# Kernel tuning notes

Measured on AMD Instinct MI355X. Metric: run time of the kernel, lower is better.

The kernel has to match this reference:

```python
import jax, jax.numpy as jnp
import numpy as np


def _safe_norm(d):
    # Euclidean norm over last axis with torch-style subgradient 0 at 0
    sq = jnp.sum(d * d, axis=-1)
    pos = sq > 0
    return jnp.where(pos, jnp.sqrt(jnp.where(pos, sq, 1.0)), 0.0)


def setup_inputs() -> dict:
    key = jax.random.key(0)
    k1, k2 = jax.random.split(key)
    B, n = 8, 256
    src = jax.random.uniform(k1, (B, n, 2), dtype=jnp.float32) * 2.0 - 1.0
    dst = jax.random.uniform(k2, (B, n, 2), dtype=jnp.float32) * 2.0 - 1.0
    return {"src": src, "dst": dst, "s": 256}


def reference(src, dst, s):
    B, n, _ = src.shape
    dt = src.dtype
    # evaluation grid, matching torch.meshgrid(indexing='ij') then stack((ix,iy))
    lin = jnp.linspace(-1.0, 1.0, s, dtype=dt)
    iy, ix = jnp.meshgrid(lin, lin, indexing="ij")
    gs = jnp.stack((ix, iy), axis=2).reshape(1, -1, 2)  # (1, s*s, 2)

    # TPS system: L wv = rhs
    delta = src[:, :, None, :] - src[:, None, :, :]          # (B,n,n,2)
    K = _safe_norm(delta)                                     # (B,n,n)
    P = jnp.concatenate([jnp.ones((B, n, 1), dt), src], 2)    # (B,n,3)
    top = jnp.concatenate([K, P], 2)                          # (B,n,n+3)
    bot = jnp.concatenate([jnp.swapaxes(P, 1, 2),
                           jnp.zeros((B, 3, 3), dt)], 2)      # (B,3,n+3)
    L = jnp.concatenate([top, bot], 1)                        # (B,n+3,n+3)
    rhs = jnp.concatenate([dst, jnp.zeros((B, 3, 2), dt)], 1) # (B,n+3,2)
    wv = jnp.linalg.solve(L, rhs)                             # (B,n+3,2)

    # evaluate warp on the grid
    S = s * s
    dg = gs[:, :, None, :] - src[:, None, :, :]               # (B,S,n,2)
    Kg = _safe_norm(dg)                                       # (B,S,n)
    gsb = jnp.broadcast_to(gs, (B, S, 2))
    Pg = jnp.concatenate([jnp.ones((B, S, 1), dt), gsb], 2)   # (B,S,3)
    Lg = jnp.concatenate([Kg, Pg], 2)                         # (B,S,n+3)
    out = jnp.matmul(Lg, wv)                                  # (B,S,2)
    return out.reshape(B, s, s, 2).transpose(0, 3, 1, 2)
```

## Files before the change

### kernel.cpp

```cpp
#include <hip/hip_runtime.h>
#include <math.h>

#define NCTRL 256
#define NA    259
#define NAUG  261
#define APITCH 264
#define BATCH 8
#define SGRID 256
#define NB    32
#define NPAN  9
#define PPITCH 36

__global__ __launch_bounds__(256) void build_kernel(const float* __restrict__ src,
                                                    const float* __restrict__ dst,
                                                    float* __restrict__ A){
  const int b = blockIdx.x / 13;
  const int s = blockIdx.x - b*13;
  const int r0 = s*20;
  const int r1 = (r0 + 20 < NA) ? r0 + 20 : NA;
  const float* sb = src + b*NCTRL*2;
  const float* db = dst + b*NCTRL*2;
  float* Ab = A + (size_t)b*NA*APITCH;
  __shared__ float sx[NCTRL], sy[NCTRL];
  {
    int t = threadIdx.x;
    float2 v = ((const float2*)sb)[t];
    sx[t] = v.x; sy[t] = v.y;
  }
  __syncthreads();
  const int total = (r1 - r0)*APITCH;
  for (int idx = threadIdx.x; idx < total; idx += 256){
    int r = r0 + idx / APITCH;
    int c = idx % APITCH;
    float v = 0.0f;
    if (r < NCTRL){
      if (c < NCTRL){
        float dx = sx[r] - sx[c];
        float dy = sy[r] - sy[c];
        v = sqrtf(fmaf(dx, dx, dy*dy));
      } else if (c == NCTRL)   v = 1.0f;
      else if (c == NCTRL+1)   v = sx[r];
      else if (c == NCTRL+2)   v = sy[r];
      else if (c == NA)        v = db[2*r];
      else if (c == NA+1)      v = db[2*r+1];
    } else if (c < NCTRL){
      v = (r == NCTRL) ? 1.0f : ((r == NCTRL+1) ? sx[c] : sy[c]);
    }
    Ab[(size_t)r*APITCH + c] = v;
  }
}

template<int NBC, int NW>
__device__ __forceinline__ void panel_ministeps(
    float (&rr)[NBC], int& org, const int rows,
    const int tid, const int lane, const int wid,
    float (*redrow)[NW][PPITCH], float (*jrow)[PPITCH],
    float (*redv)[NW], int (*redi)[NW], int (*redo_)[NW], int* jorg)
{
  #pragma unroll
  for (int j = 0; j < NBC; ++j){
    const int par = j & 1;
    float bv = (tid >= j && tid < rows) ? fabsf(rr[j]) : -1.0f;
    int bi = tid;
    #pragma unroll
    for (int off = 32; off; off >>= 1){
      float ov = __shfl_xor(bv, off);
      int   oi = __shfl_xor(bi, off);
      if (ov > bv || (ov == bv && oi < bi)){ bv = ov; bi = oi; }
    }
    if (tid == bi){
      redv[par][wid] = bv; redi[par][wid] = bi; redo_[par][wid] = org;
      if (bv >= 0.0f){
        if (NBC == NB){
          #pragma unroll
          for (int q = 0; q < 8; ++q){
            float4 v; v.x=rr[4*q]; v.y=rr[4*q+1]; v.z=rr[4*q+2]; v.w=rr[4*q+3];
            *(float4*)&redrow[par][wid][4*q] = v;
          }
        } else {
          #pragma unroll
          for (int c = 0; c < NBC; ++c) redrow[par][wid][c] = rr[c];
        }
      }
    }
    if (tid == j){
      jorg[par] = org;
      if (NBC == NB){
        #pragma unroll
        for (int q = 0; q < 8; ++q){
          float4 v; v.x=rr[4*q]; v.y=rr[4*q+1]; v.z=rr[4*q+2]; v.w=rr[4*q+3];
          *(float4*)&jrow[par][4*q] = v;
        }
      } else {
        #pragma unroll
        for (int c = 0; c < NBC; ++c) jrow[par][c] = rr[c];
      }
    }
    __syncthreads();
    float gv = redv[par][0]; int gw = 0;
    #pragma unroll
    for (int w = 1; w < NW; ++w){
      if (redv[par][w] > gv ||
          (redv[par][w] == gv && redi[par][w] < redi[par][gw])){
        gv = redv[par][w]; gw = w;
      }
    }
    const int gbi  = redi[par][gw];
    const int gorg = redo_[par][gw];
    float pr[NBC];
    if (NBC == NB){
      #pragma unroll
      for (int q = 0; q < 8; ++q){
        float4 v = *(const float4*)&redrow[par][gw][4*q];
        pr[4*q]=v.x; pr[4*q+1]=v.y; pr[4*q+2]=v.z; pr[4*q+3]=v.w;
      }
    } else {
      #pragma unroll
      for (int c = 0; c < NBC; ++c) pr[c] = redrow[par][gw][c];
    }
    if (gbi != j){
      if (tid == j){
        #pragma unroll
        for (int c = 0; c < NBC; ++c) rr[c] = pr[c];
        org = gorg;
      } else if (tid == gbi){
        #pragma unroll
        for (int c = 0; c < NBC; ++c) rr[c] = jrow[par][c];
        org = jorg[par];
      }
    }
    if (tid > j && tid < rows){
      const float rpiv = 1.0f / pr[j];
      float f = rr[j] * rpiv;
      rr[j] = f;
      #pragma unroll
      for (int c = j+1; c < NBC; ++c) rr[c] = fmaf(-f, pr[c], rr[c]);
    }
  }
}

template<int NBC>
__global__ __launch_bounds__(320) void panel_kernel(float* __restrict__ A,
                                                    int* __restrict__ permbuf,
                                                    int k0, int pidx){
  const int b = blockIdx.x;
  float* Ab = A + (size_t)b*NA*APITCH;
  const int tid  = threadIdx.x;
  const int lane = tid & 63;
  const int wid  = tid >> 6;
  const int rows = NA - k0;

  __shared__ float pan[NA][PPITCH];
  __shared__ float redrow[2][5][PPITCH];
  __shared__ float jrow[2][PPITCH];
  __shared__ float redv[2][5];
  __shared__ int   redi[2][5], redo_[2][5];
  __shared__ int   jorg[2];

  for (int idx = tid; idx < rows*8; idx += 320){
    int i = idx >> 3, q = idx & 7;
    *(float4*)&pan[i][4*q] =
      *(const float4*)(Ab + (size_t)(k0+i)*APITCH + k0 + 4*q);
  }
  __syncthreads();

  float rr[NBC];
  int org = tid;
  if (tid < rows){
    #pragma unroll
    for (int q = 0; q < 8; ++q){
      float4 v = *(const float4*)&pan[tid][4*q];
      rr[4*q]=v.x; rr[4*q+1]=v.y; rr[4*q+2]=v.z; rr[4*q+3]=v.w;
    }
  } else {
    #pragma unroll
    for (int c = 0; c < NBC; ++c) rr[c] = 0.0f;
  }

  panel_ministeps<NBC,5>(rr, org, rows, tid, lane, wid,
                         redrow, jrow, redv, redi, redo_, jorg);

  if (tid < rows){
    #pragma unroll
    for (int q = 0; q < 8; ++q){
      float4 v; v.x=rr[4*q]; v.y=rr[4*q+1]; v.z=rr[4*q+2]; v.w=rr[4*q+3];
      *(float4*)&pan[tid][4*q] = v;
    }
    permbuf[b*(NPAN*NA) + pidx*NA + tid] = org;
  }
  __syncthreads();
  for (int idx = tid; idx < rows*8; idx += 320){
    int i = idx >> 3, q = idx & 7;
    *(float4*)(Ab + (size_t)(k0+i)*APITCH + k0 + 4*q) = *(const float4*)&pan[i][4*q];
  }
}

template<int NBC, int NBCN, bool LOOK>
__global__ __launch_bounds__(256) void update_kernel(float* __restrict__ A,
                                                     int* __restrict__ permbuf,
                                                     int k0, int pidx, int sb){
  const int rows = NA - k0;
  const int ctop = k0 + NBC;
  const int tc   = NAUG - ctop;
  const int b    = blockIdx.x / sb;
  const int s    = blockIdx.x - b*sb;
  const int c0   = s*32;
  const int W    = (tc - c0 < 32) ? (tc - c0) : 32;
  float* Ab = A + (size_t)b*NA*APITCH;
  const int tid  = threadIdx.x;
  const int lane = tid & 63;
  const int wid  = tid >> 6;

  __shared__ float pan[NA][PPITCH];
  __shared__ float stage[NA][PPITCH];
  __shared__ float ustg[NB][PPITCH];
  __shared__ int   perm[NA];
  __shared__ float redrowL[2][4][PPITCH];
  __shared__ float jrowL[2][PPITCH];
  __shared__ float redvL[2][4];
  __shared__ int   rediL[2][4], redoL[2][4];
  __shared__ int   jorgL[2];

  for (int i = tid; i < rows; i += 256)
    perm[i] = permbuf[b*(NPAN*NA) + pidx*NA + i];
  if (NBC == NB){
    for (int idx = tid; idx < rows*8; idx += 256){
      int i = idx >> 3, q = idx & 7;
      *(float4*)&pan[i][4*q] =
        *(const float4*)(Ab + (size_t)(k0+i)*APITCH + k0 + 4*q);
    }
  } else {
    for (int idx = tid; idx < rows*NBC; idx += 256){
      int i = idx / NBC, c = idx - i*NBC;
      pan[i][c] = Ab[(size_t)(k0+i)*APITCH + k0 + c];
    }
  }
  __syncthreads();

  for (int idx = tid; idx < rows*W; idx += 256){
    int i = idx / W, c = idx - i*W;
    stage[i][c] = Ab[(size_t)(k0+perm[i])*APITCH + ctop + c0 + c];
  }
  __syncthreads();

  if (tid < W){
    float u[NBC];
    #pragma unroll
    for (int m = 0; m < NBC; ++m) u[m] = stage[m][tid];
    #pragma unroll
    for (int m = 0; m < NBC; ++m){
      #pragma unroll
      for (int jj = m+1; jj < NBC; ++jj)
        u[jj] = fmaf(-pan[jj][m], u[m], u[jj]);
    }
    #pragma unroll
    for (int m = 0; m < NBC; ++m){
      ustg[m][tid] = u[m];
      Ab[(size_t)(k0+m)*APITCH + ctop + c0 + tid] = u[m];
    }
  }
  __syncthreads();

  const int R = rows - NBC;
  if (R > 0){
    const int rt = (R + 3) >> 2, ct = (W + 3) >> 2;
    for (int t = tid; t < rt*ct; t += 256){
      int tr = t / ct, tcc = t - tr*ct;
      int i0 = tr*4, cc0 = tcc*4;
      const bool full = (cc0 + 4 <= W);
      int ir[4];
      #pragma unroll
      for (int r = 0; r < 4; ++r){
        int i = i0 + r;
        ir[r] = (i < R) ? i : (R - 1);
      }
      float acc[4][4];
      #pragma unroll
      for (int r = 0; r < 4; ++r){
        if (full){
          float4 v = *(const float4*)&stage[NBC + ir[r]][cc0];
          acc[r][0]=v.x; acc[r][1]=v.y; acc[r][2]=v.z; acc[r][3]=v.w;
        } else {
          #pragma unroll
          for (int c = 0; c < 4; ++c)
            acc[r][c] = (cc0 + c < W) ? stage[NBC + ir[r]][cc0 + c] : 0.0f;
        }
      }
      if (NBC == NB){
        #pragma unroll
        for (int mq = 0; mq < NBC/4; ++mq){
          float4 lv[4];
          #pragma unroll
          for (int r = 0; r < 4; ++r)
            lv[r] = *(const float4*)&pan[NBC + ir[r]][4*mq];
          #pragma unroll
          for (int mi = 0; mi < 4; ++mi){
            float4 uv = *(const float4*)&ustg[4*mq + mi][cc0];
            #pragma unroll
            for (int r = 0; r < 4; ++r){
              float l = (mi==0) ? lv[r].x : (mi==1) ? lv[r].y : (mi==2) ? lv[r].z : lv[r].w;
              acc[r][0] = fmaf(-l, uv.x, acc[r][0]);
              acc[r][1] = fmaf(-l, uv.y, acc[r][1]);
              acc[r][2] = fmaf(-l, uv.z, acc[r][2]);
              acc[r][3] = fmaf(-l, uv.w, acc[r][3]);
            }
          }
        }
      } else {
        #pragma unroll
        for (int mi = 0; mi < NBC; ++mi){
          #pragma unroll
          for (int r = 0; r < 4; ++r){
            float l = pan[NBC + ir[r]][mi];
            #pragma unroll
            for (int c = 0; c < 4; ++c)
              acc[r][c] = fmaf(-l, ustg[mi][cc0 + c], acc[r][c]);
          }
        }
      }
      #pragma unroll
      for (int r = 0; r < 4; ++r){
        if (i0 + r < R){
          float* g = Ab + (size_t)(k0 + NBC + i0 + r)*APITCH + ctop + c0 + cc0;
          if (full){
            float4 v; v.x=acc[r][0]; v.y=acc[r][1]; v.z=acc[r][2]; v.w=acc[r][3];
            *(float4*)g = v;
            if (LOOK && s == 0) *(float4*)&stage[NBC + i0 + r][cc0] = v;
          } else {
            #pragma unroll
            for (int c = 0; c < 4; ++c)
              if (cc0 + c < W){
                g[c] = acc[r][c];
                if (LOOK && s == 0) stage[NBC + i0 + r][cc0 + c] = acc[r][c];
              }
          }
        }
      }
    }
  }

  if (LOOK && s == 0){
    __syncthreads();
    const int k0n   = k0 + NBC;
    const int rowsN = rows - NBC;
    float rr[NBCN];
    int org = tid;
    if (tid < rowsN){
      #pragma unroll
      for (int c = 0; c < NBCN; ++c) rr[c] = stage[NBC + tid][c];
    } else {
      #pragma unroll
      for (int c = 0; c < NBCN; ++c) rr[c] = 0.0f;
    }
    panel_ministeps<NBCN,4>(rr, org, rowsN, tid, lane, wid,
                            redrowL, jrowL, redvL, rediL, redoL, jorgL);
    if (tid < rowsN){
      #pragma unroll
      for (int c = 0; c < NBCN; ++c) stage[NBC + tid][c] = rr[c];
      permbuf[b*(NPAN*NA) + (pidx+1)*NA + tid] = org;
    }
    __syncthreads();
    if (NBCN == NB){
      for (int idx = tid; idx < rowsN*8; idx += 256){
        int i = idx >> 3, q = idx & 7;
        *(float4*)(Ab + (size_t)(k0n+i)*APITCH + k0n + 4*q) =
          *(const float4*)&stage[NBC + i][4*q];
      }
    } else {
      for (int idx = tid; idx < rowsN*NBCN; idx += 256){
        int i = idx / NBCN, c = idx - i*NBCN;
        Ab[(size_t)(k0n+i)*APITCH + k0n + c] = stage[NBC + i][c];
      }
    }
  }
}

__global__ __launch_bounds__(512) void backsub_kernel(const float* __restrict__ A,
                                                      float* __restrict__ wv){
  const int b = blockIdx.x;
  const float* Ab = A + (size_t)b*NA*APITCH;
  const int tid  = threadIdx.x;
  const int lane = tid & 63;
  const int wid  = tid >> 6;

  __shared__ float t2[NA][2];
  __shared__ float xs[NA][2];
  __shared__ float u11[NB][NB+1];

  for (int i = tid; i < NA; i += 512){
    t2[i][0] = Ab[(size_t)i*APITCH + NA];
    t2[i][1] = Ab[(size_t)i*APITCH + NA + 1];
  }
  __syncthreads();

  for (int bp = NPAN-1; bp >= 0; --bp){
    const int k0 = bp*NB;
    const int nb = (NA - k0 < NB) ? (NA - k0) : NB;

    for (int idx = tid; idx < nb*nb; idx += 512){
      int r = idx / nb, c = idx - r*nb;
      u11[r][c] = Ab[(size_t)(k0+r)*APITCH + k0 + c];
    }
    __syncthreads();

    if (wid == 0){
      int j = lane >> 1, ch = lane & 1;
      float tval = (j < nb) ? t2[k0+j][ch] : 0.0f;
      for (int k = nb-1; k >= 0; --k){
        float tk = __shfl(tval, 2*k + ch);
        float xk = tk / u11[k][k];
        if (j <  k) tval = fmaf(-u11[j][k], xk, tval);
        if (j == k) tval = xk;
      }
      if (j < nb) xs[k0+j][ch] = tval;
    }
    __syncthreads();

    if (nb == NB){
      const int q = tid & 7;
      for (int base = 0; base < k0; base += 64){
        const int i = base + (tid >> 3);
        float px = 0.0f, py = 0.0f;
        if (i < k0){
          float4 v = *(const float4*)(Ab + (size_t)i*APITCH + k0 + 4*q);
          px = v.x*xs[k0+4*q+0][0] + v.y*xs[k0+4*q+1][0]
             + v.z*xs[k0+4*q+2][0] + v.w*xs[k0+4*q+3][0];
          py = v.x*xs[k0+4*q+0][1] + v.y*xs[k0+4*q+1][1]
             + v.z*xs[k0+4*q+2][1] + v.w*xs[k0+4*q+3][1];
        }
        px += __shfl_xor(px, 1); px += __shfl_xor(px, 2); px += __shfl_xor(px, 4);
        py += __shfl_xor(py, 1); py += __shfl_xor(py, 2); py += __shfl_xor(py, 4);
        if (q == 0 && i < k0){
          t2[i][0] -= px;
          t2[i][1] -= py;
        }
      }
    } else {
      for (int i = tid; i < k0; i += 512){
        float s0 = 0.0f, s1 = 0.0f;
        #pragma unroll
        for (int m = 0; m < 3; ++m){
          float u = Ab[(size_t)i*APITCH + k0 + m];
          s0 = fmaf(u, xs[k0+m][0], s0);
          s1 = fmaf(u, xs[k0+m][1], s1);
        }
        t2[i][0] -= s0;
        t2[i][1] -= s1;
      }
    }
    __syncthreads();
  }

  for (int i = tid; i < NA; i += 512){
    wv[((size_t)b*NA + i)*2 + 0] = xs[i][0];
    wv[((size_t)b*NA + i)*2 + 1] = xs[i][1];
  }
}

__global__ __launch_bounds__(256) void eval_kernel(const float* __restrict__ src,
                                                   const float* __restrict__ wv,
                                                   float* __restrict__ out){
  const int b  = blockIdx.x >> 8;
  const int yi = blockIdx.x & 255;
  const int xi = threadIdx.x;
  __shared__ float2 sxy[NCTRL], wxy[NCTRL];
  const float* sb = src + b*NCTRL*2;
  const float* wb = wv + (size_t)b*NA*2;
  sxy[xi] = ((const float2*)sb)[xi];
  wxy[xi] = ((const float2*)wb)[xi];
  __syncthreads();

  const float step = 2.0f/255.0f;
  const float gx = -1.0f + step*(float)xi;
  const float gy = -1.0f + step*(float)yi;

  float accx = wb[512] + wb[514]*gx + wb[516]*gy;
  float accy = wb[513] + wb[515]*gx + wb[517]*gy;

  #pragma unroll 8
  for (int j = 0; j < NCTRL; ++j){
    float2 s = sxy[j];
    float2 w = wxy[j];
    float dx = gx - s.x;
    float dy = gy - s.y;
    float r = sqrtf(fmaf(dx, dx, dy*dy));
    accx = fmaf(r, w.x, accx);
    accy = fmaf(r, w.y, accy);
  }
  out[((size_t)(b*2    )*SGRID + yi)*SGRID + xi] = accx;
  out[((size_t)(b*2 + 1)*SGRID + yi)*SGRID + xi] = accy;
}

extern "C" void kernel_launch(void* const* d_in, const int* in_sizes, int n_in,
                              void* d_out, int out_size, void* d_ws, size_t ws_size,
                              hipStream_t stream) {
  const float* src = (const float*)d_in[0];
  const float* dst = (const float*)d_in[1];
  float* out = (float*)d_out;

  const size_t matElems = (size_t)BATCH*NA*APITCH;
  float* A     = (float*)d_ws;
  float* wv    = A + matElems;
  int*   permb = (int*)(wv + (size_t)BATCH*NA*2);

  build_kernel<<<BATCH*13, 256, 0, stream>>>(src, dst, A);

  panel_kernel<NB><<<BATCH, 320, 0, stream>>>(A, permb, 0, 0);

  for (int p = 0; p <= 6; ++p){
    const int k0 = p*NB;
    const int tc = NAUG - (k0 + NB);
    const int sb = (tc + 31) >> 5;
    update_kernel<NB, NB, true><<<BATCH*sb, 256, 0, stream>>>(A, permb, k0, p, sb);
  }
  update_kernel<NB, 3, true><<<BATCH, 256, 0, stream>>>(A, permb, 7*NB, 7, 1);
  update_kernel<3, 3, false><<<BATCH, 256, 0, stream>>>(A, permb, 8*NB, 8, 1);

  backsub_kernel<<<BATCH, 512, 0, stream>>>(A, wv);
  eval_kernel<<<BATCH*SGRID, 256, 0, stream>>>(src, wv, out);
}
```

Baseline: 595.4 us.

## Fuse build with first panel, move panel factorization to LDS, tile eval rows

Merges matrix construction and the first panel LU into one kernel, and rewrites the panel mini-step engine to operate on shared-memory rows instead of register arrays. The final 3-column panel is folded into the last lookahead update, which drops a launch. The eval kernel now computes four grid rows per thread, reusing dx and the control-point loads, and uses the hardware sqrt builtin. Together these cut launches and per-point ALU work. The costs are a single-block-per-batch build, so construction is less parallel, and extra LDS traffic in the panel loop.

```diff
diff --git a/kernel.cpp b/kernel.cpp
--- a/kernel.cpp
+++ b/kernel.cpp
@@ -10,57 +10,18 @@
 #define NB    32
 #define NPAN  9
 #define PPITCH 36
-
-__global__ __launch_bounds__(256) void build_kernel(const float* __restrict__ src,
-                                                    const float* __restrict__ dst,
-                                                    float* __restrict__ A){
-  const int b = blockIdx.x / 13;
-  const int s = blockIdx.x - b*13;
-  const int r0 = s*20;
-  const int r1 = (r0 + 20 < NA) ? r0 + 20 : NA;
-  const float* sb = src + b*NCTRL*2;
-  const float* db = dst + b*NCTRL*2;
-  float* Ab = A + (size_t)b*NA*APITCH;
-  __shared__ float sx[NCTRL], sy[NCTRL];
-  {
-    int t = threadIdx.x;
-    float2 v = ((const float2*)sb)[t];
-    sx[t] = v.x; sy[t] = v.y;
-  }
-  __syncthreads();
-  const int total = (r1 - r0)*APITCH;
-  for (int idx = threadIdx.x; idx < total; idx += 256){
-    int r = r0 + idx / APITCH;
-    int c = idx % APITCH;
-    float v = 0.0f;
-    if (r < NCTRL){
-      if (c < NCTRL){
-        float dx = sx[r] - sx[c];
-        float dy = sy[r] - sy[c];
-        v = sqrtf(fmaf(dx, dx, dy*dy));
-      } else if (c == NCTRL)   v = 1.0f;
-      else if (c == NCTRL+1)   v = sx[r];
-      else if (c == NCTRL+2)   v = sy[r];
-      else if (c == NA)        v = db[2*r];
-      else if (c == NA+1)      v = db[2*r+1];
-    } else if (c < NCTRL){
-      v = (r == NCTRL) ? 1.0f : ((r == NCTRL+1) ? sx[c] : sy[c]);
-    }
-    Ab[(size_t)r*APITCH + c] = v;
-  }
-}
-
-template<int NBC, int NW>
-__device__ __forceinline__ void panel_ministeps(
-    float (&rr)[NBC], int& org, const int rows,
+#define PY    4
+
+template<int NW>
+__device__ __forceinline__ void panel_lds_engine(
+    float (*rowbase)[PPITCH], const int rows, const int nb, int& org,
     const int tid, const int lane, const int wid,
     float (*redrow)[NW][PPITCH], float (*jrow)[PPITCH],
     float (*redv)[NW], int (*redi)[NW], int (*redo_)[NW], int* jorg)
 {
-  #pragma unroll
-  for (int j = 0; j < NBC; ++j){
+  for (int j = 0; j < nb; ++j){
     const int par = j & 1;
-    float bv = (tid >= j && tid < rows) ? fabsf(rr[j]) : -1.0f;
+    float bv = (tid >= j && tid < rows) ? fabsf(rowbase[tid][j]) : -1.0f;
     int bi = tid;
     #pragma unroll
     for (int off = 32; off; off >>= 1){
@@ -70,31 +31,15 @@
     }
     if (tid == bi){
       redv[par][wid] = bv; redi[par][wid] = bi; redo_[par][wid] = org;
-      if (bv >= 0.0f){
-        if (NBC == NB){
-          #pragma unroll
-          for (int q = 0; q < 8; ++q){
-            float4 v; v.x=rr[4*q]; v.y=rr[4*q+1]; v.z=rr[4*q+2]; v.w=rr[4*q+3];
-            *(float4*)&redrow[par][wid][4*q] = v;
-          }
-        } else {
-          #pragma unroll
-          for (int c = 0; c < NBC; ++c) redrow[par][wid][c] = rr[c];
-        }
-      }
+      #pragma unroll
+      for (int q = 0; q < 8; ++q)
+        *(float4*)&redrow[par][wid][4*q] = *(const float4*)&rowbase[tid][4*q];
     }
     if (tid == j){
       jorg[par] = org;
-      if (NBC == NB){
-        #pragma unroll
-        for (int q = 0; q < 8; ++q){
-          float4 v; v.x=rr[4*q]; v.y=rr[4*q+1]; v.z=rr[4*q+2]; v.w=rr[4*q+3];
-          *(float4*)&jrow[par][4*q] = v;
-        }
-      } else {
-        #pragma unroll
-        for (int c = 0; c < NBC; ++c) jrow[par][c] = rr[c];
-      }
+      #pragma unroll
+      for (int q = 0; q < 8; ++q)
+        *(float4*)&jrow[par][4*q] = *(const float4*)&rowbase[tid][4*q];
     }
     __syncthreads();
     float gv = redv[par][0]; int gw = 0;
@@ -105,102 +50,112 @@
         gv = redv[par][w]; gw = w;
       }
     }
-    const int gbi  = redi[par][gw];
-    const int gorg = redo_[par][gw];
-    float pr[NBC];
-    if (NBC == NB){
-      #pragma unroll
-      for (int q = 0; q < 8; ++q){
-        float4 v = *(const float4*)&redrow[par][gw][4*q];
-        pr[4*q]=v.x; pr[4*q+1]=v.y; pr[4*q+2]=v.z; pr[4*q+3]=v.w;
-      }
-    } else {
-      #pragma unroll
-      for (int c = 0; c < NBC; ++c) pr[c] = redrow[par][gw][c];
-    }
+    const int gbi = redi[par][gw];
+    const float* pvrow = redrow[par][gw];
     if (gbi != j){
       if (tid == j){
         #pragma unroll
-        for (int c = 0; c < NBC; ++c) rr[c] = pr[c];
-        org = gorg;
+        for (int q = 0; q < 8; ++q)
+          *(float4*)&rowbase[j][4*q] = *(const float4*)&pvrow[4*q];
+        org = redo_[par][gw];
       } else if (tid == gbi){
         #pragma unroll
-        for (int c = 0; c < NBC; ++c) rr[c] = jrow[par][c];
+        for (int q = 0; q < 8; ++q)
+          *(float4*)&rowbase[gbi][4*q] = *(const float4*)&jrow[par][4*q];
         org = jorg[par];
       }
     }
     if (tid > j && tid < rows){
-      const float rpiv = 1.0f / pr[j];
-      float f = rr[j] * rpiv;
-      rr[j] = f;
-      #pragma unroll
-      for (int c = j+1; c < NBC; ++c) rr[c] = fmaf(-f, pr[c], rr[c]);
-    }
-  }
-}
-
-template<int NBC>
-__global__ __launch_bounds__(320) void panel_kernel(float* __restrict__ A,
-                                                    int* __restrict__ permbuf,
-                                                    int k0, int pidx){
+      const float piv = pvrow[j];
+      float f = rowbase[tid][j] / piv;
+      rowbase[tid][j] = f;
+      const int q0 = (j+1) >> 2;
+      {
+        float4 a = *(float4*)&rowbase[tid][4*q0];
+        float4 pv = *(const float4*)&pvrow[4*q0];
+        if (4*q0+0 > j) a.x = fmaf(-f, pv.x, a.x);
+        if (4*q0+1 > j) a.y = fmaf(-f, pv.y, a.y);
+        if (4*q0+2 > j) a.z = fmaf(-f, pv.z, a.z);
+        if (4*q0+3 > j) a.w = fmaf(-f, pv.w, a.w);
+        *(float4*)&rowbase[tid][4*q0] = a;
+      }
+      for (int q = q0+1; q < 8; ++q){
+        float4 a = *(float4*)&rowbase[tid][4*q];
+        float4 pv = *(const float4*)&pvrow[4*q];
+        a.x = fmaf(-f, pv.x, a.x); a.y = fmaf(-f, pv.y, a.y);
+        a.z = fmaf(-f, pv.z, a.z); a.w = fmaf(-f, pv.w, a.w);
+        *(float4*)&rowbase[tid][4*q] = a;
+      }
+    }
+  }
+}
+
+__global__ __launch_bounds__(320) void build_panel0(const float* __restrict__ src,
+                                                    const float* __restrict__ dst,
+                                                    float* __restrict__ A,
+                                                    int* __restrict__ permbuf){
   const int b = blockIdx.x;
   float* Ab = A + (size_t)b*NA*APITCH;
   const int tid  = threadIdx.x;
   const int lane = tid & 63;
   const int wid  = tid >> 6;
-  const int rows = NA - k0;
 
   __shared__ float pan[NA][PPITCH];
   __shared__ float redrow[2][5][PPITCH];
   __shared__ float jrow[2][PPITCH];
   __shared__ float redv[2][5];
-  __shared__ int   redi[2][5], redo_[2][5];
-  __shared__ int   jorg[2];
-
-  for (int idx = tid; idx < rows*8; idx += 320){
+  __shared__ int   redi[2][5], redo_[2][5], jorg[2];
+  __shared__ float sx[NCTRL], sy[NCTRL];
+
+  if (tid < NCTRL){
+    float2 v = ((const float2*)(src + b*NCTRL*2))[tid];
+    sx[tid] = v.x; sy[tid] = v.y;
+  }
+  __syncthreads();
+  {
+    const float* db = dst + b*NCTRL*2;
+    for (int idx = tid; idx < NA*APITCH; idx += 320){
+      int r = idx / APITCH;
+      int c = idx - r*APITCH;
+      float v = 0.0f;
+      if (r < NCTRL){
+        if (c < NCTRL){
+          float dx = sx[r] - sx[c];
+          float dy = sy[r] - sy[c];
+          v = __builtin_amdgcn_sqrtf(fmaf(dx, dx, dy*dy));
+        } else if (c == NCTRL)   v = 1.0f;
+        else if (c == NCTRL+1)   v = sx[r];
+        else if (c == NCTRL+2)   v = sy[r];
+        else if (c == NA)        v = db[2*r];
+        else if (c == NA+1)      v = db[2*r+1];
+      } else if (c < NCTRL){
+        v = (r == NCTRL) ? 1.0f : ((r == NCTRL+1) ? sx[c] : sy[c]);
+      }
+      Ab[idx] = v;
+      if (c < NB) pan[r][c] = v;
+    }
+  }
+  __syncthreads();
+
+  int org = tid;
+  panel_lds_engine<5>(pan, NA, NB, org, tid, lane, wid,
+                      redrow, jrow, redv, redi, redo_, jorg);
+
+  if (tid < NA) permbuf[b*(NPAN*NA) + tid] = org;
+  __syncthreads();
+  for (int idx = tid; idx < NA*8; idx += 320){
     int i = idx >> 3, q = idx & 7;
-    *(float4*)&pan[i][4*q] =
-      *(const float4*)(Ab + (size_t)(k0+i)*APITCH + k0 + 4*q);
-  }
-  __syncthreads();
-
-  float rr[NBC];
-  int org = tid;
-  if (tid < rows){
-    #pragma unroll
-    for (int q = 0; q < 8; ++q){
-      float4 v = *(const float4*)&pan[tid][4*q];
-      rr[4*q]=v.x; rr[4*q+1]=v.y; rr[4*q+2]=v.z; rr[4*q+3]=v.w;
-    }
-  } else {
-    #pragma unroll
-    for (int c = 0; c < NBC; ++c) rr[c] = 0.0f;
-  }
-
-  panel_ministeps<NBC,5>(rr, org, rows, tid, lane, wid,
-                         redrow, jrow, redv, redi, redo_, jorg);
-
-  if (tid < rows){
-    #pragma unroll
-    for (int q = 0; q < 8; ++q){
-      float4 v; v.x=rr[4*q]; v.y=rr[4*q+1]; v.z=rr[4*q+2]; v.w=rr[4*q+3];
-      *(float4*)&pan[tid][4*q] = v;
-    }
-    permbuf[b*(NPAN*NA) + pidx*NA + tid] = org;
-  }
-  __syncthreads();
-  for (int idx = tid; idx < rows*8; idx += 320){
-    int i = idx >> 3, q = idx & 7;
-    *(float4*)(Ab + (size_t)(k0+i)*APITCH + k0 + 4*q) = *(const float4*)&pan[i][4*q];
-  }
-}
-
-template<int NBC, int NBCN, bool LOOK>
+    *(float4*)(Ab + (size_t)i*APITCH + 4*q) = *(const float4*)&pan[i][4*q];
+  }
+}
+
+template<bool LOOK>
 __global__ __launch_bounds__(256) void update_kernel(float* __restrict__ A,
                                                      int* __restrict__ permbuf,
-                                                     int k0, int pidx, int sb){
+                                                     int k0, int pidx, int sb,
+                                                     int nbn, int wbw){
   const int rows = NA - k0;
-  const int ctop = k0 + NBC;
+  const int ctop = k0 + NB;
   const int tc   = NAUG - ctop;
   const int b    = blockIdx.x / sb;
   const int s    = blockIdx.x - b*sb;
@@ -215,25 +170,17 @@
   __shared__ float stage[NA][PPITCH];
   __shared__ float ustg[NB][PPITCH];
   __shared__ int   perm[NA];
-  __shared__ float redrowL[2][4][PPITCH];
-  __shared__ float jrowL[2][PPITCH];
-  __shared__ float redvL[2][4];
-  __shared__ int   rediL[2][4], redoL[2][4];
-  __shared__ int   jorgL[2];
+  __shared__ float redrow[2][4][PPITCH];
+  __shared__ float jrow[2][PPITCH];
+  __shared__ float redv[2][4];
+  __shared__ int   redi[2][4], redo_[2][4], jorg[2];
 
   for (int i = tid; i < rows; i += 256)
     perm[i] = permbuf[b*(NPAN*NA) + pidx*NA + i];
-  if (NBC == NB){
-    for (int idx = tid; idx < rows*8; idx += 256){
-      int i = idx >> 3, q = idx & 7;
-      *(float4*)&pan[i][4*q] =
-        *(const float4*)(Ab + (size_t)(k0+i)*APITCH + k0 + 4*q);
-    }
-  } else {
-    for (int idx = tid; idx < rows*NBC; idx += 256){
-      int i = idx / NBC, c = idx - i*NBC;
-      pan[i][c] = Ab[(size_t)(k0+i)*APITCH + k0 + c];
-    }
+  for (int idx = tid; idx < rows*8; idx += 256){
+    int i = idx >> 3, q = idx & 7;
+    *(float4*)&pan[i][4*q] =
+      *(const float4*)(Ab + (size_t)(k0+i)*APITCH + k0 + 4*q);
   }
   __syncthreads();
 
@@ -244,24 +191,24 @@
   __syncthreads();
 
   if (tid < W){
-    float u[NBC];
-    #pragma unroll
-    for (int m = 0; m < NBC; ++m) u[m] = stage[m][tid];
-    #pragma unroll
-    for (int m = 0; m < NBC; ++m){
-      #pragma unroll
-      for (int jj = m+1; jj < NBC; ++jj)
+    float u[NB];
+    #pragma unroll
+    for (int m = 0; m < NB; ++m) u[m] = stage[m][tid];
+    #pragma unroll
+    for (int m = 0; m < NB; ++m){
+      #pragma unroll
+      for (int jj = m+1; jj < NB; ++jj)
         u[jj] = fmaf(-pan[jj][m], u[m], u[jj]);
     }
     #pragma unroll
-    for (int m = 0; m < NBC; ++m){
+    for (int m = 0; m < NB; ++m){
       ustg[m][tid] = u[m];
       Ab[(size_t)(k0+m)*APITCH + ctop + c0 + tid] = u[m];
     }
   }
   __syncthreads();
 
-  const int R = rows - NBC;
+  const int R = rows - NB;
   if (R > 0){
     const int rt = (R + 3) >> 2, ct = (W + 3) >> 2;
     for (int t = tid; t < rt*ct; t += 256){
@@ -278,60 +225,47 @@
       #pragma unroll
       for (int r = 0; r < 4; ++r){
         if (full){
-          float4 v = *(const float4*)&stage[NBC + ir[r]][cc0];
+          float4 v = *(const float4*)&stage[NB + ir[r]][cc0];
           acc[r][0]=v.x; acc[r][1]=v.y; acc[r][2]=v.z; acc[r][3]=v.w;
         } else {
           #pragma unroll
           for (int c = 0; c < 4; ++c)
-            acc[r][c] = (cc0 + c < W) ? stage[NBC + ir[r]][cc0 + c] : 0.0f;
-        }
-      }
-      if (NBC == NB){
+            acc[r][c] = (cc0 + c < W) ? stage[NB + ir[r]][cc0 + c] : 0.0f;
+        }
+      }
+      #pragma unroll
+      for (int mq = 0; mq < NB/4; ++mq){
+        float4 lv[4];
         #pragma unroll
-        for (int mq = 0; mq < NBC/4; ++mq){
-          float4 lv[4];
-          #pragma unroll
-          for (int r = 0; r < 4; ++r)
-            lv[r] = *(const float4*)&pan[NBC + ir[r]][4*mq];
-          #pragma unroll
-          for (int mi = 0; mi < 4; ++mi){
-            float4 uv = *(const float4*)&ustg[4*mq + mi][cc0];
-            #pragma unroll
-            for (int r = 0; r < 4; ++r){
-              float l = (mi==0) ? lv[r].x : (mi==1) ? lv[r].y : (mi==2) ? lv[r].z : lv[r].w;
-              acc[r][0] = fmaf(-l, uv.x, acc[r][0]);
-              acc[r][1] = fmaf(-l, uv.y, acc[r][1]);
-              acc[r][2] = fmaf(-l, uv.z, acc[r][2]);
-              acc[r][3] = fmaf(-l, uv.w, acc[r][3]);
-            }
-          }
-        }
-      } else {
+        for (int r = 0; r < 4; ++r)
+          lv[r] = *(const float4*)&pan[NB + ir[r]][4*mq];
         #pragma unroll
-        for (int mi = 0; mi < NBC; ++mi){
+        for (int mi = 0; mi < 4; ++mi){
+          float4 uv = *(const float4*)&ustg[4*mq + mi][cc0];
           #pragma unroll
           for (int r = 0; r < 4; ++r){
-            float l = pan[NBC + ir[r]][mi];
-            #pragma unroll
-            for (int c = 0; c < 4; ++c)
-              acc[r][c] = fmaf(-l, ustg[mi][cc0 + c], acc[r][c]);
+            float l = (mi==0) ? lv[r].x : (mi==1) ? lv[r].y : (mi==2) ? lv[r].z : lv[r].w;
+            acc[r][0] = fmaf(-l, uv.x, acc[r][0]);
+            acc[r][1] = fmaf(-l, uv.y, acc[r][1]);
+            acc[r][2] = fmaf(-l, uv.z, acc[r][2]);
+            acc[r][3] = fmaf(-l, uv.w, acc[r][3]);
           }
         }
       }
       #pragma unroll
       for (int r = 0; r < 4; ++r){
         if (i0 + r < R){
-          float* g = Ab + (size_t)(k0 + NBC + i0 + r)*APITCH + ctop + c0 + cc0;
+          float* g = Ab + (size_t)(k0 + NB + i0 + r)*APITCH + ctop + c0 + cc0;
           if (full){
             float4 v; v.x=acc[r][0]; v.y=acc[r][1]; v.z=acc[r][2]; v.w=acc[r][3];
             *(float4*)g = v;
-            if (LOOK && s == 0) *(float4*)&stage[NBC + i0 + r][cc0] = v;
+            if (LOOK && s == 0) *(float4*)&stage[NB + i0 + r][cc0] = v;
           } else {
             #pragma unroll
             for (int c = 0; c < 4; ++c)
               if (cc0 + c < W){
                 g[c] = acc[r][c];
-                if (LOOK && s == 0) stage[NBC + i0 + r][cc0 + c] = acc[r][c];
+                if (LOOK && s == 0) stage[NB + i0 + r][cc0 + c] = acc[r][c];
               }
           }
         }
@@ -341,35 +275,23 @@
 
   if (LOOK && s == 0){
     __syncthreads();
-    const int k0n   = k0 + NBC;
-    const int rowsN = rows - NBC;
-    float rr[NBCN];
+    const int k0n   = k0 + NB;
+    const int rowsN = rows - NB;
     int org = tid;
-    if (tid < rowsN){
-      #pragma unroll
-      for (int c = 0; c < NBCN; ++c) rr[c] = stage[NBC + tid][c];
-    } else {
-      #pragma unroll
-      for (int c = 0; c < NBCN; ++c) rr[c] = 0.0f;
-    }
-    panel_ministeps<NBCN,4>(rr, org, rowsN, tid, lane, wid,
-                            redrowL, jrowL, redvL, rediL, redoL, jorgL);
-    if (tid < rowsN){
-      #pragma unroll
-      for (int c = 0; c < NBCN; ++c) stage[NBC + tid][c] = rr[c];
-      permbuf[b*(NPAN*NA) + (pidx+1)*NA + tid] = org;
-    }
-    __syncthreads();
-    if (NBCN == NB){
+    panel_lds_engine<4>(&stage[NB], rowsN, nbn, org, tid, lane, wid,
+                        redrow, jrow, redv, redi, redo_, jorg);
+    if (tid < rowsN) permbuf[b*(NPAN*NA) + (pidx+1)*NA + tid] = org;
+    __syncthreads();
+    if (wbw == NB){
       for (int idx = tid; idx < rowsN*8; idx += 256){
         int i = idx >> 3, q = idx & 7;
         *(float4*)(Ab + (size_t)(k0n+i)*APITCH + k0n + 4*q) =
-          *(const float4*)&stage[NBC + i][4*q];
+          *(const float4*)&stage[NB + i][4*q];
       }
     } else {
-      for (int idx = tid; idx < rowsN*NBCN; idx += 256){
-        int i = idx / NBCN, c = idx - i*NBCN;
-        Ab[(size_t)(k0n+i)*APITCH + k0n + c] = stage[NBC + i][c];
+      for (int idx = tid; idx < rowsN*wbw; idx += 256){
+        int i = idx / wbw, c = idx - i*wbw;
+        Ab[(size_t)(k0n+i)*APITCH + k0n + c] = stage[NB + i][c];
       }
     }
   }
@@ -460,35 +382,52 @@
 __global__ __launch_bounds__(256) void eval_kernel(const float* __restrict__ src,
                                                    const float* __restrict__ wv,
                                                    float* __restrict__ out){
-  const int b  = blockIdx.x >> 8;
-  const int yi = blockIdx.x & 255;
+  const int b  = blockIdx.x >> 6;
+  const int yg = blockIdx.x & 63;
   const int xi = threadIdx.x;
-  __shared__ float2 sxy[NCTRL], wxy[NCTRL];
+  __shared__ float4 cw[NCTRL];
   const float* sb = src + b*NCTRL*2;
   const float* wb = wv + (size_t)b*NA*2;
-  sxy[xi] = ((const float2*)sb)[xi];
-  wxy[xi] = ((const float2*)wb)[xi];
+  {
+    float2 sv = ((const float2*)sb)[xi];
+    float2 wv2 = ((const float2*)wb)[xi];
+    cw[xi] = make_float4(sv.x, sv.y, wv2.x, wv2.y);
+  }
   __syncthreads();
 
   const float step = 2.0f/255.0f;
   const float gx = -1.0f + step*(float)xi;
-  const float gy = -1.0f + step*(float)yi;
-
-  float accx = wb[512] + wb[514]*gx + wb[516]*gy;
-  float accy = wb[513] + wb[515]*gx + wb[517]*gy;
-
-  #pragma unroll 8
+  const float w0x = wb[512], w1x = wb[514], w2x = wb[516];
+  const float w0y = wb[513], w1y = wb[515], w2y = wb[517];
+
+  float gy[PY], ax[PY], ay[PY];
+  #pragma unroll
+  for (int p = 0; p < PY; ++p){
+    gy[p] = -1.0f + step*(float)(yg*PY + p);
+    ax[p] = w0x + w1x*gx + w2x*gy[p];
+    ay[p] = w0y + w1y*gx + w2y*gy[p];
+  }
+
+  #pragma unroll 4
   for (int j = 0; j < NCTRL; ++j){
-    float2 s = sxy[j];
-    float2 w = wxy[j];
-    float dx = gx - s.x;
-    float dy = gy - s.y;
-    float r = sqrtf(fmaf(dx, dx, dy*dy));
-    accx = fmaf(r, w.x, accx);
-    accy = fmaf(r, w.y, accy);
-  }
-  out[((size_t)(b*2    )*SGRID + yi)*SGRID + xi] = accx;
-  out[((size_t)(b*2 + 1)*SGRID + yi)*SGRID + xi] = accy;
+    float4 c = cw[j];
+    float dx = gx - c.x;
+    float dx2 = dx*dx;
+    #pragma unroll
+    for (int p = 0; p < PY; ++p){
+      float dy = gy[p] - c.y;
+      float r = __builtin_amdgcn_sqrtf(fmaf(dy, dy, dx2));
+      ax[p] = fmaf(r, c.z, ax[p]);
+      ay[p] = fmaf(r, c.w, ay[p]);
+    }
+  }
+
+  const int y0 = yg*PY;
+  #pragma unroll
+  for (int p = 0; p < PY; ++p){
+    out[((size_t)(b*2    )*SGRID + y0 + p)*SGRID + xi] = ax[p];
+    out[((size_t)(b*2 + 1)*SGRID + y0 + p)*SGRID + xi] = ay[p];
+  }
 }
 
 extern "C" void kernel_launch(void* const* d_in, const int* in_sizes, int n_in,
@@ -503,19 +442,16 @@
   float* wv    = A + matElems;
   int*   permb = (int*)(wv + (size_t)BATCH*NA*2);
 
-  build_kernel<<<BATCH*13, 256, 0, stream>>>(src, dst, A);
-
-  panel_kernel<NB><<<BATCH, 320, 0, stream>>>(A, permb, 0, 0);
+  build_panel0<<<BATCH, 320, 0, stream>>>(src, dst, A, permb);
 
   for (int p = 0; p <= 6; ++p){
     const int k0 = p*NB;
     const int tc = NAUG - (k0 + NB);
     const int sb = (tc + 31) >> 5;
-    update_kernel<NB, NB, true><<<BATCH*sb, 256, 0, stream>>>(A, permb, k0, p, sb);
-  }
-  update_kernel<NB, 3, true><<<BATCH, 256, 0, stream>>>(A, permb, 7*NB, 7, 1);
-  update_kernel<3, 3, false><<<BATCH, 256, 0, stream>>>(A, permb, 8*NB, 8, 1);
+    update_kernel<true><<<BATCH*sb, 256, 0, stream>>>(A, permb, k0, p, sb, NB, NB);
+  }
+  update_kernel<true><<<BATCH, 256, 0, stream>>>(A, permb, 7*NB, 7, 1, 3, 5);
 
   backsub_kernel<<<BATCH, 512, 0, stream>>>(A, wv);
-  eval_kernel<<<BATCH*SGRID, 256, 0, stream>>>(src, wv, out);
-}
+  eval_kernel<<<BATCH*(SGRID/PY), 256, 0, stream>>>(src, wv, out);
+}
```

Result: slower. 677.6 us (+13.8%).
